# Kernel tuning notes

Hardware: AMD Instinct MI355X
Metric: run time of the kernel (lower is better)

Reference implementation:

```python
import jax, jax.numpy as jnp
import numpy as np

B, N, C = 8, 8192, 64
P, K = 2048, 16
C_IN = 2 * C + 6   # 134: concat(diff, center) of (feat ++ xyz)
H1, H2 = 64, 128
EPS = 1e-5


def setup_inputs() -> dict:
    key = jax.random.key(0)
    ks = jax.random.split(key, 16)
    inp = {
        "xyz": jax.random.normal(ks[0], (B, N, 3), dtype=jnp.float32),
        "feat": jax.random.normal(ks[1], (B, C, N), dtype=jnp.float32),
        # SharedMLP layer 1: 1x1 conv + BN(eval) + ReLU
        "W1": jax.random.normal(ks[2], (H1, C_IN), dtype=jnp.float32) * (1.0 / np.sqrt(C_IN)),
        "b1": jnp.zeros((H1,), dtype=jnp.float32),
        "g1": jax.random.uniform(ks[3], (H1,), minval=0.5, maxval=1.5, dtype=jnp.float32),
        "be1": jax.random.normal(ks[4], (H1,), dtype=jnp.float32) * 0.1,
        "m1": jax.random.normal(ks[5], (H1,), dtype=jnp.float32) * 0.1,
        "v1": jax.random.uniform(ks[6], (H1,), minval=0.5, maxval=1.5, dtype=jnp.float32),
        # SharedMLP layer 2
        "W2": jax.random.normal(ks[7], (H2, H1), dtype=jnp.float32) * (1.0 / np.sqrt(H1)),
        "b2": jnp.zeros((H2,), dtype=jnp.float32),
        "g2": jax.random.uniform(ks[8], (H2,), minval=0.5, maxval=1.5, dtype=jnp.float32),
        "be2": jax.random.normal(ks[9], (H2,), dtype=jnp.float32) * 0.1,
        "m2": jax.random.normal(ks[10], (H2,), dtype=jnp.float32) * 0.1,
        "v2": jax.random.uniform(ks[11], (H2,), minval=0.5, maxval=1.5, dtype=jnp.float32),
        "npoints": P,
    }
    return inp


def _mlp_layer(x, W, b, g, be, m, v):
    # x: [b,p,k,cin] -> 1x1 conv (einsum) + eval-mode BN + ReLU
    y = jnp.einsum("bpkc,oc->bpko", x, W) + b
    y = g * (y - m) * jax.lax.rsqrt(v + EPS) + be
    return jax.nn.relu(y)


def reference(xyz, feat, W1, b1, g1, be1, m1, v1, W2, b2, g2, be2, m2, v2, npoints):
    p = npoints
    # Range sampling: take first p points
    new_xyz = xyz[:, :p]                       # [b,p,3]
    feat_t = jnp.swapaxes(feat, 1, 2)          # [b,n,c]
    feat_x = jnp.concatenate([feat_t, xyz], axis=-1)   # [b,n,c+3] (use_xyz)
    new_feat_x = feat_x[:, :p]                 # [b,p,c+3]
    # KNN via squared euclidean distance, expanded form to avoid [b,p,n,3]
    sq_q = jnp.sum(new_xyz * new_xyz, axis=-1)           # [b,p]
    sq_r = jnp.sum(xyz * xyz, axis=-1)                   # [b,n]
    dots = jnp.einsum("bpd,bnd->bpn", new_xyz, xyz)      # [b,p,n]
    d2 = sq_q[:, :, None] + sq_r[:, None, :] - 2.0 * dots
    _, idx = jax.lax.top_k(-d2, K)             # [b,p,k] nearest (ascending dist)
    # Gather neighbor features: [b,p,k,c+3]
    knn_feat = jax.vmap(lambda f, i: f[i])(feat_x, idx)
    tiled = jnp.broadcast_to(new_feat_x[:, :, None, :], knn_feat.shape)
    edge = jnp.concatenate([knn_feat - tiled, tiled], axis=-1)  # [b,p,k,2c+6]
    h = _mlp_layer(edge, W1, b1, g1, be1, m1, v1)
    h = _mlp_layer(h, W2, b2, g2, be2, m2, v2)              # [b,p,k,H2]
    new_feat = jnp.swapaxes(jnp.max(h, axis=2), 1, 2)       # [b,H2,p]
    sample_idx = jnp.broadcast_to(jnp.arange(p, dtype=jnp.int32), (xyz.shape[0], p))
    return new_xyz, new_feat, sample_idx
```

## Files before the change

### kernel.cpp

```cpp
#include <hip/hip_runtime.h>
#include <hip/hip_bf16.h>

#define BB 8
#define NN 8192
#define CC 64
#define PP 2048
#define KK 16
#define H1 64
#define H2 128
#define K1PAD 160
#define K2PAD 72

typedef float  f32x4 __attribute__((ext_vector_type(4)));
typedef short  s16x8 __attribute__((ext_vector_type(8)));

#define OFF_FXT   0u
#define OFF_PTS4  17825792u
#define OFF_KNN   19922944u
#define OFF_W1P   20971520u
#define OFF_W2P   20992000u
#define OFF_C1    21010432u
#define OFF_C2    21010688u

#define FLTMAX 3.402823466e+38f

static __device__ __forceinline__ unsigned short bf16b(float v) {
    __hip_bfloat16 h = __float2bfloat16(v);
    return *reinterpret_cast<unsigned short*>(&h);
}
static __device__ __forceinline__ unsigned pk2(float a, float b) {
    return ((unsigned)bf16b(b) << 16) | (unsigned)bf16b(a);
}
#define LDS_FENCE() asm volatile("s_waitcnt lgkmcnt(0)" ::: "memory")

__global__ void k0_weights(const float* __restrict__ W1, const float* __restrict__ b1,
                           const float* __restrict__ g1, const float* __restrict__ be1,
                           const float* __restrict__ m1, const float* __restrict__ v1,
                           const float* __restrict__ W2, const float* __restrict__ b2,
                           const float* __restrict__ g2, const float* __restrict__ be2,
                           const float* __restrict__ m2, const float* __restrict__ v2,
                           unsigned short* __restrict__ w1p, unsigned short* __restrict__ w2p,
                           float* __restrict__ c1, float* __restrict__ c2) {
    int i = blockIdx.x * 256 + threadIdx.x;
    if (i < 64 * K1PAD) {
        int n = i / K1PAD, c = i - n * K1PAD;
        float s = g1[n] * rsqrtf(v1[n] + 1e-5f);
        float val = 0.f;
        if (c < 67)                 val = W1[n * 134 + c] * s;
        else if (c >= 72 && c < 139) val = W1[n * 134 + (c - 5)] * s;
        w1p[i] = bf16b(val);
    }
    int j = i - 64 * K1PAD;
    if (j >= 0 && j < 128 * K2PAD) {
        int o = j / K2PAD, k = j - o * K2PAD;
        float s = g2[o] * rsqrtf(v2[o] + 1e-5f);
        w2p[j] = bf16b((k < 64) ? W2[o * 64 + k] * s : 0.f);
    }
    int l = i - (64 * K1PAD + 128 * K2PAD);
    if (l >= 0 && l < 64) {
        float s = g1[l] * rsqrtf(v1[l] + 1e-5f);
        c1[l] = s * (b1[l] - m1[l]) + be1[l];
    }
    int p = l - 64;
    if (p >= 0 && p < 128) {
        float s = g2[p] * rsqrtf(v2[p] + 1e-5f);
        c2[p] = s * (b2[p] - m2[p]) + be2[p];
    }
}

__global__ __launch_bounds__(512) void k1_prep(const float* __restrict__ xyz,
                                               const float* __restrict__ feat,
                                               float* __restrict__ fxt,
                                               float4* __restrict__ pts4,
                                               float* __restrict__ out0,
                                               float* __restrict__ out2) {
    __shared__ float tile[68][65];
    int b  = blockIdx.x >> 7;
    int n0 = (blockIdx.x & 127) * 64;
    int tx = threadIdx.x & 63, ty = threadIdx.x >> 6;
    for (int c = ty; c < 68; c += 8) {
        float v;
        if (c < 64)       v = feat[((size_t)b * 64 + c) * NN + n0 + tx];
        else if (c < 67)  v = xyz[((size_t)b * NN + n0 + tx) * 3 + (c - 64)];
        else              v = 0.f;
        tile[c][tx] = v;
    }
    __syncthreads();
    size_t base = ((size_t)b * NN + n0) * 68;
    for (int e = threadIdx.x; e < 64 * 68; e += 512) {
        int nl = e / 68, c = e - nl * 68;
        fxt[base + e] = tile[c][nl];
    }
    if (threadIdx.x < 64) {
        int n = n0 + threadIdx.x;
        float x = tile[64][threadIdx.x], y = tile[65][threadIdx.x], z = tile[66][threadIdx.x];
        pts4[(size_t)b * NN + n] = make_float4(x, y, z, x * x + y * y + z * z);
        if (n0 < PP) out2[b * PP + n] = (float)n;
    }
    if (n0 < PP) {
        for (int e = threadIdx.x; e < 64 * 3; e += 512) {
            int nl = e / 3, d = e - nl * 3;
            out0[((size_t)b * PP + n0 + nl) * 3 + d] = tile[64 + d][nl];
        }
    }
}

__global__ __launch_bounds__(1024, 4) void k2_knn(const float4* __restrict__ pts4,
                                                  int* __restrict__ knn) {
    __shared__ float4 stage[8192];
    __shared__ float2 scratch[16][2][64];
    int lane = threadIdx.x & 63;
    int wv   = threadIdx.x >> 6;
    int b    = blockIdx.x >> 5;
    int q0   = (blockIdx.x & 31) * 64 + wv * 4;
    size_t pb = (size_t)b * NN;

    float4 qc = make_float4(0.f, 0.f, 0.f, 0.f);
    if (lane < 4) qc = pts4[pb + q0 + lane];
    float qx2 = -2.f * qc.x, qy2 = -2.f * qc.y, qz2 = -2.f * qc.z;
    float bx[4], by[4], bz[4];
#pragma unroll
    for (int q = 0; q < 4; ++q) {
        bx[q] = __shfl(qx2, q); by[q] = __shfl(qy2, q); bz[q] = __shfl(qz2, q);
    }

#pragma unroll
    for (int i = 0; i < 8; ++i) {
        int p = i * 1024 + threadIdx.x;
        float4 v = pts4[pb + p];
        int r = p >> 6, c = p & 63;
        stage[(r << 6) | ((c + (r >> 1)) & 63)] = v;
    }
    __syncthreads();

    float m[4];
#pragma unroll
    for (int q = 0; q < 4; ++q) m[q] = FLTMAX;
#pragma unroll
    for (int rr = 0; rr < 2; ++rr) {
        int rowbase = (2 * lane + rr) << 6;
#pragma unroll
        for (int j8 = 0; j8 < 8; ++j8) {
            float4 cc[8];
#pragma unroll
            for (int i = 0; i < 8; ++i)
                cc[i] = stage[rowbase | ((j8 * 8 + i + lane) & 63)];
#pragma unroll
            for (int q = 0; q < 4; ++q) {
                float x = bx[q], y = by[q], z = bz[q];
#pragma unroll
                for (int i = 0; i < 8; i += 2) {
                    float e0 = fmaf(z, cc[i].z, fmaf(y, cc[i].y, fmaf(x, cc[i].x, cc[i].w)));
                    float e1 = fmaf(z, cc[i+1].z, fmaf(y, cc[i+1].y, fmaf(x, cc[i+1].x, cc[i+1].w)));
                    m[q] = fminf(fminf(m[q], e0), e1);
                }
            }
        }
    }

    float sv0 = m[0], sv1 = m[1], sv2 = m[2], sv3 = m[3];
#pragma unroll
    for (int k = 2; k <= 64; k <<= 1) {
#pragma unroll
        for (int j = k >> 1; j > 0; j >>= 1) {
            bool keepMin = (((lane & k) == 0) == ((lane & j) == 0));
            float p0 = __shfl_xor(sv0, j, 64);
            float p1 = __shfl_xor(sv1, j, 64);
            float p2 = __shfl_xor(sv2, j, 64);
            float p3 = __shfl_xor(sv3, j, 64);
            sv0 = keepMin ? fminf(sv0, p0) : fmaxf(sv0, p0);
            sv1 = keepMin ? fminf(sv1, p1) : fmaxf(sv1, p1);
            sv2 = keepMin ? fminf(sv2, p2) : fmaxf(sv2, p2);
            sv3 = keepMin ? fminf(sv3, p3) : fmaxf(sv3, p3);
        }
    }
    float T[4];
    T[0] = __shfl(sv0, 15, 64); T[1] = __shfl(sv1, 15, 64);
    T[2] = __shfl(sv2, 15, 64); T[3] = __shfl(sv3, 15, 64);

    unsigned long long below = (lane == 63) ? 0x7FFFFFFFFFFFFFFFull
                                            : ((1ull << lane) - 1ull);
#pragma unroll
    for (int pr = 0; pr < 4; pr += 2) {
        float kd[2]; int kn[2];
#pragma unroll
        for (int u = 0; u < 2; ++u) {
            int q = pr + u;
            float x = bx[q], y = by[q], z = bz[q], tq = T[q];
            unsigned long long rm = __ballot(m[q] <= tq);
            int cnt = 0;
            while (rm) {
                int sl = __ffsll((long long)rm) - 1; rm &= rm - 1;
                int phys = (lane + sl) & 63;
                float4 c0 = stage[((2 * sl) << 6) | phys];
                float4 c1 = stage[((2 * sl + 1) << 6) | phys];
                float e0 = fmaf(z, c0.z, fmaf(y, c0.y, fmaf(x, c0.x, c0.w)));
                float e1 = fmaf(z, c1.z, fmaf(y, c1.y, fmaf(x, c1.x, c1.w)));
                unsigned long long b0 = __ballot(e0 <= tq);
                if (e0 <= tq) {
                    int pos = cnt + __popcll(b0 & below);
                    if (pos < 64)
                        scratch[wv][u][pos] = make_float2(e0, __int_as_float(sl * 128 + lane));
                }
                cnt += __popcll(b0);
                unsigned long long b1 = __ballot(e1 <= tq);
                if (e1 <= tq) {
                    int pos = cnt + __popcll(b1 & below);
                    if (pos < 64)
                        scratch[wv][u][pos] = make_float2(e1, __int_as_float(sl * 128 + 64 + lane));
                }
                cnt += __popcll(b1);
            }
            LDS_FENCE();
            int M = min(cnt, 64);
            float2 kv = scratch[wv][u][lane];
            kd[u] = (lane < M) ? kv.x : FLTMAX;
            kn[u] = (lane < M) ? __float_as_int(kv.y) : 0x7FFFFFFF;
        }
#pragma unroll
        for (int k = 2; k <= 64; k <<= 1) {
#pragma unroll
            for (int j = k >> 1; j > 0; j >>= 1) {
                bool takeMin = (((lane & k) == 0) == ((lane & j) == 0));
                float pd0 = __shfl_xor(kd[0], j, 64); int pn0 = __shfl_xor(kn[0], j, 64);
                float pd1 = __shfl_xor(kd[1], j, 64); int pn1 = __shfl_xor(kn[1], j, 64);
                bool l0 = (pd0 < kd[0]) || (pd0 == kd[0] && pn0 < kn[0]);
                bool s0 = takeMin ? l0 : !l0;
                kd[0] = s0 ? pd0 : kd[0]; kn[0] = s0 ? pn0 : kn[0];
                bool l1 = (pd1 < kd[1]) || (pd1 == kd[1] && pn1 < kn[1]);
                bool s1 = takeMin ? l1 : !l1;
                kd[1] = s1 ? pd1 : kd[1]; kn[1] = s1 ? pn1 : kn[1];
            }
        }
        if (lane < 16) {
            knn[((size_t)(b * PP + q0 + pr)) * KK + lane]     = kn[0];
            knn[((size_t)(b * PP + q0 + pr + 1)) * KK + lane] = kn[1];
        }
        LDS_FENCE();
    }
}

__global__ __launch_bounds__(64, 2) void k3_mlp(const float* __restrict__ fxt,
                                                const int* __restrict__ knn,
                                                const unsigned short* __restrict__ w1p,
                                                const unsigned short* __restrict__ w2p,
                                                const float* __restrict__ c1,
                                                const float* __restrict__ c2,
                                                float* __restrict__ out1) {
    __shared__ __align__(16) char seg[8192];
    int lane = threadIdx.x;
    int wg   = blockIdx.x;
    float4* sh_t4 = (float4*)(seg + 7424);
    unsigned* sh_tbd = (unsigned*)(seg + 7696);
    unsigned short* h1l = (unsigned short*)(seg + 5120);
    const float4* fx4 = (const float4*)fxt;

    int col = lane & 15, quad = lane >> 4;
    int r = lane >> 2, s = lane & 3;

    s16x8 w1f[5][4];
#pragma unroll
    for (int ks = 0; ks < 5; ++ks)
#pragma unroll
        for (int nt = 0; nt < 4; ++nt)
            w1f[ks][nt] = *(const s16x8*)(w1p + (nt * 16 + col) * K1PAD + ks * 32 + quad * 8);
    s16x8 w2f[2][8];
#pragma unroll
    for (int ks = 0; ks < 2; ++ks)
#pragma unroll
        for (int nt = 0; nt < 8; ++nt)
            w2f[ks][nt] = *(const s16x8*)(w2p + (nt * 16 + col) * K2PAD + ks * 32 + quad * 8);
    float c1v[4], c2v[8];
#pragma unroll
    for (int nt = 0; nt < 4; ++nt) c1v[nt] = c1[nt * 16 + col];
#pragma unroll
    for (int nt = 0; nt < 8; ++nt) c2v[nt] = c2[nt * 16 + col];

    int idxA = knn[wg * 16 + (lane >> 4) * 32768 + (lane & 15)];
    int idxB = knn[wg * 16 + 131072 + (lane >> 4) * 32768 + (lane & 15)];

    float4 cc[2][5];
    float4 tv[2];

#define PREFETCH(buf, it_) {                                                  \
        size_t bb_ = (size_t)(it_) * NN;                                      \
        tv[buf] = make_float4(0.f, 0.f, 0.f, 0.f);                            \
        if (lane < 17) tv[buf] = fx4[(bb_ + wg) * 17 + lane];                 \
        int nidx_ = __shfl(((it_) < 4) ? idxA : idxB, ((it_) & 3) * 16 + r, 64); \
        const float4* rowp_ = fx4 + (bb_ + nidx_) * 17;                       \
        cc[buf][0] = rowp_[s];      cc[buf][1] = rowp_[4 + s];                \
        cc[buf][2] = rowp_[8 + s];  cc[buf][3] = rowp_[12 + s];               \
        cc[buf][4] = rowp_[16];  }

    PREFETCH(0, 0);

#pragma unroll 2
    for (int it = 0; it < 8; ++it) {
        int cur = it & 1, nxt = cur ^ 1;
        if (lane < 17) {
            float4 v = tv[cur];
            sh_t4[lane] = v;
            sh_tbd[lane * 2]     = pk2(v.x, v.y);
            sh_tbd[lane * 2 + 1] = pk2(v.z, v.w);
        }
        LDS_FENCE();
        char* erow = seg + r * 320;
#pragma unroll
        for (int j = 0; j < 4; ++j) {
            int c4 = j * 4 + s;
            float4 v = cc[cur][j], t = sh_t4[c4];
            *(unsigned*)(erow + c4 * 8)     = pk2(v.x - t.x, v.y - t.y);
            *(unsigned*)(erow + c4 * 8 + 4) = pk2(v.z - t.z, v.w - t.w);
        }
        if (s == 0) {
            float4 v = cc[cur][4], t = sh_t4[16];
            *(unsigned*)(erow + 128) = pk2(v.x - t.x, v.y - t.y);
            *(unsigned*)(erow + 132) = pk2(v.z - t.z, v.w - t.w);
        }
        for (int j = s; j < 34; j += 4)
            *(unsigned*)(erow + 144 + j * 4) = sh_tbd[j];
#pragma unroll
        for (int j = s; j < 12; j += 4) {
            int w = (j < 2) ? (34 + j) : (68 + j);
            *(unsigned*)(erow + w * 4) = 0u;
        }
        if (it < 7) PREFETCH(nxt, it + 1);
        LDS_FENCE();
        f32x4 acc1[4];
#pragma unroll
        for (int nt = 0; nt < 4; ++nt) acc1[nt] = (f32x4){0.f, 0.f, 0.f, 0.f};
#pragma unroll
        for (int ks = 0; ks < 5; ++ks) {
            s16x8 a = *(const s16x8*)(seg + col * 320 + ks * 64 + quad * 16);
#pragma unroll
            for (int nt = 0; nt < 4; ++nt)
                acc1[nt] = __builtin_amdgcn_mfma_f32_16x16x32_bf16(a, w1f[ks][nt], acc1[nt], 0, 0, 0);
        }
#pragma unroll
        for (int nt = 0; nt < 4; ++nt) {
#pragma unroll
            for (int rr = 0; rr < 4; ++rr) {
                float y = fmaxf(acc1[nt][rr] + c1v[nt], 0.f);
                h1l[(quad * 4 + rr) * K2PAD + nt * 16 + col] = bf16b(y);
            }
        }
        LDS_FENCE();
        f32x4 acc2[8];
#pragma unroll
        for (int nt = 0; nt < 8; ++nt) acc2[nt] = (f32x4){0.f, 0.f, 0.f, 0.f};
#pragma unroll
        for (int ks = 0; ks < 2; ++ks) {
            s16x8 a = *(const s16x8*)(seg + 5120 + col * 144 + ks * 64 + quad * 16);
#pragma unroll
            for (int nt = 0; nt < 8; ++nt)
                acc2[nt] = __builtin_amdgcn_mfma_f32_16x16x32_bf16(a, w2f[ks][nt], acc2[nt], 0, 0, 0);
        }
#pragma unroll
        for (int nt = 0; nt < 8; ++nt) {
            float m0 = fmaxf(fmaxf(acc2[nt][0], acc2[nt][1]), fmaxf(acc2[nt][2], acc2[nt][3]));
            m0 = m0 + c2v[nt];
            m0 = fmaxf(m0, 0.f);
            m0 = fmaxf(m0, __shfl_xor(m0, 16, 64));
            m0 = fmaxf(m0, __shfl_xor(m0, 32, 64));
            if (quad == 0)
                out1[((size_t)it * H2 + nt * 16 + col) * PP + wg] = m0;
        }
    }
#undef PREFETCH
}

extern "C" void kernel_launch(void* const* d_in, const int* in_sizes, int n_in,
                              void* d_out, int out_size, void* d_ws, size_t ws_size,
                              hipStream_t stream) {
    const float* xyz  = (const float*)d_in[0];
    const float* feat = (const float*)d_in[1];
    const float* W1   = (const float*)d_in[2];
    const float* b1   = (const float*)d_in[3];
    const float* g1   = (const float*)d_in[4];
    const float* be1  = (const float*)d_in[5];
    const float* m1   = (const float*)d_in[6];
    const float* v1   = (const float*)d_in[7];
    const float* W2   = (const float*)d_in[8];
    const float* b2   = (const float*)d_in[9];
    const float* g2   = (const float*)d_in[10];
    const float* be2  = (const float*)d_in[11];
    const float* m2   = (const float*)d_in[12];
    const float* v2   = (const float*)d_in[13];

    char* ws = (char*)d_ws;
    float*          fxt  = (float*)(ws + OFF_FXT);
    float4*         pts4 = (float4*)(ws + OFF_PTS4);
    int*            knn  = (int*)(ws + OFF_KNN);
    unsigned short* w1p  = (unsigned short*)(ws + OFF_W1P);
    unsigned short* w2p  = (unsigned short*)(ws + OFF_W2P);
    float*          c1   = (float*)(ws + OFF_C1);
    float*          c2   = (float*)(ws + OFF_C2);

    float* out0 = (float*)d_out;
    float* out1 = out0 + (size_t)BB * PP * 3;
    float* out2 = out1 + (size_t)BB * H2 * PP;

    hipLaunchKernelGGL(k0_weights, dim3(77), dim3(256), 0, stream,
                       W1, b1, g1, be1, m1, v1, W2, b2, g2, be2, m2, v2,
                       w1p, w2p, c1, c2);
    hipLaunchKernelGGL(k1_prep, dim3(1024), dim3(512), 0, stream,
                       xyz, feat, fxt, pts4, out0, out2);
    hipLaunchKernelGGL(k2_knn, dim3(256), dim3(1024), 0, stream, pts4, knn);
    hipLaunchKernelGGL(k3_mlp, dim3(2048), dim3(64), 0, stream,
                       fxt, knn, w1p, w2p, c1, c2, out1);
}
```

Baseline: 185.6 us.

## Restructure MLP kernel into 4-wave blocks with coalesced LDS-staged output

The MLP kernel now runs 256-thread blocks in which each wave handles 4 consecutive queries of one batch, instead of 64-thread blocks that process one query index across all 8 batches. Per-query outputs are staged in an LDS tile and written as contiguous 16-float runs per channel, replacing the earlier strided single-float stores. The zero padding of the edge and hidden tiles is hoisted out of the loop so it is written once per wave. The trade-offs are more LDS per block and an added block-level barrier, while weights are still loaded into registers once per wave, now amortized over 4 queries instead of 8.

```diff
diff --git a/kernel.cpp b/kernel.cpp
--- a/kernel.cpp
+++ b/kernel.cpp
@@ -240,16 +240,21 @@
     }
 }
 
-__global__ __launch_bounds__(64, 2) void k3_mlp(const float* __restrict__ fxt,
-                                                const int* __restrict__ knn,
-                                                const unsigned short* __restrict__ w1p,
-                                                const unsigned short* __restrict__ w2p,
-                                                const float* __restrict__ c1,
-                                                const float* __restrict__ c2,
-                                                float* __restrict__ out1) {
-    __shared__ __align__(16) char seg[8192];
-    int lane = threadIdx.x;
-    int wg   = blockIdx.x;
+__global__ __launch_bounds__(256, 4) void k3_mlp(const float* __restrict__ fxt,
+                                                 const int* __restrict__ knn,
+                                                 const unsigned short* __restrict__ w1p,
+                                                 const unsigned short* __restrict__ w2p,
+                                                 const float* __restrict__ c1,
+                                                 const float* __restrict__ c2,
+                                                 float* __restrict__ out1) {
+    __shared__ __align__(16) char smem[4 * 7936];
+    __shared__ float otile[16][132];
+    int lane = threadIdx.x & 63;
+    int wv   = threadIdx.x >> 6;
+    int b    = blockIdx.x >> 7;
+    int qg   = blockIdx.x & 127;
+    int qbase = qg * 16;
+    char* seg = smem + wv * 7936;
     float4* sh_t4 = (float4*)(seg + 7424);
     unsigned* sh_tbd = (unsigned*)(seg + 7696);
     unsigned short* h1l = (unsigned short*)(seg + 5120);
@@ -258,6 +263,17 @@
     int col = lane & 15, quad = lane >> 4;
     int r = lane >> 2, s = lane & 3;
 
+#pragma unroll
+    for (int i = lane; i < 192; i += 64) {
+        int rr = i / 12, jj = i - rr * 12;
+        int dw = (jj < 2) ? (34 + jj) : (68 + jj);
+        *(unsigned*)(seg + rr * 320 + dw * 4) = 0u;
+    }
+    {
+        int rr = lane >> 2, dd = lane & 3;
+        *(unsigned*)(seg + 5120 + rr * 144 + 128 + dd * 4) = 0u;
+    }
+
     s16x8 w1f[5][4];
 #pragma unroll
     for (int ks = 0; ks < 5; ++ks)
@@ -276,27 +292,25 @@
 #pragma unroll
     for (int nt = 0; nt < 8; ++nt) c2v[nt] = c2[nt * 16 + col];
 
-    int idxA = knn[wg * 16 + (lane >> 4) * 32768 + (lane & 15)];
-    int idxB = knn[wg * 16 + 131072 + (lane >> 4) * 32768 + (lane & 15)];
+    int idxAll = knn[((size_t)(b * PP + qbase + wv * 4)) * KK + lane];
 
     float4 cc[2][5];
     float4 tv[2];
 
-#define PREFETCH(buf, it_) {                                                  \
-        size_t bb_ = (size_t)(it_) * NN;                                      \
+#define PREFETCH(buf, qi_) {                                                  \
+        int q_ = qbase + wv * 4 + (qi_);                                      \
         tv[buf] = make_float4(0.f, 0.f, 0.f, 0.f);                            \
-        if (lane < 17) tv[buf] = fx4[(bb_ + wg) * 17 + lane];                 \
-        int nidx_ = __shfl(((it_) < 4) ? idxA : idxB, ((it_) & 3) * 16 + r, 64); \
-        const float4* rowp_ = fx4 + (bb_ + nidx_) * 17;                       \
+        if (lane < 17) tv[buf] = fx4[((size_t)b * NN + q_) * 17 + lane];      \
+        int nidx_ = __shfl(idxAll, (qi_) * 16 + r, 64);                       \
+        const float4* rowp_ = fx4 + ((size_t)b * NN + nidx_) * 17;            \
         cc[buf][0] = rowp_[s];      cc[buf][1] = rowp_[4 + s];                \
         cc[buf][2] = rowp_[8 + s];  cc[buf][3] = rowp_[12 + s];               \
-        cc[buf][4] = rowp_[16];  }
+        cc[buf][4] = rowp_[16]; }
 
     PREFETCH(0, 0);
 
-#pragma unroll 2
-    for (int it = 0; it < 8; ++it) {
-        int cur = it & 1, nxt = cur ^ 1;
+    for (int qi = 0; qi < 4; ++qi) {
+        int cur = qi & 1, nxt = cur ^ 1;
         if (lane < 17) {
             float4 v = tv[cur];
             sh_t4[lane] = v;
@@ -319,12 +333,7 @@
         }
         for (int j = s; j < 34; j += 4)
             *(unsigned*)(erow + 144 + j * 4) = sh_tbd[j];
-#pragma unroll
-        for (int j = s; j < 12; j += 4) {
-            int w = (j < 2) ? (34 + j) : (68 + j);
-            *(unsigned*)(erow + w * 4) = 0u;
-        }
-        if (it < 7) PREFETCH(nxt, it + 1);
+        if (qi < 3) PREFETCH(nxt, qi + 1);
         LDS_FENCE();
         f32x4 acc1[4];
 #pragma unroll
@@ -363,8 +372,14 @@
             m0 = fmaxf(m0, __shfl_xor(m0, 16, 64));
             m0 = fmaxf(m0, __shfl_xor(m0, 32, 64));
             if (quad == 0)
-                out1[((size_t)it * H2 + nt * 16 + col) * PP + wg] = m0;
-        }
+                otile[wv * 4 + qi][nt * 16 + col] = m0;
+        }
+        LDS_FENCE();
+    }
+    __syncthreads();
+    for (int i = threadIdx.x; i < H2 * 16; i += 256) {
+        int ch = i >> 4, q = i & 15;
+        out1[((size_t)(b * H2 + ch)) * PP + qbase + q] = otile[q][ch];
     }
 #undef PREFETCH
 }
@@ -406,6 +421,6 @@
     hipLaunchKernelGGL(k1_prep, dim3(1024), dim3(512), 0, stream,
                        xyz, feat, fxt, pts4, out0, out2);
     hipLaunchKernelGGL(k2_knn, dim3(256), dim3(1024), 0, stream, pts4, knn);
-    hipLaunchKernelGGL(k3_mlp, dim3(2048), dim3(64), 0, stream,
+    hipLaunchKernelGGL(k3_mlp, dim3(1024), dim3(256), 0, stream,
                        fxt, knn, w1p, w2p, c1, c2, out1);
 }
```

Result: slower. 248.8 us (+34.1%).
